# Kernel tuning notes

Measured on AMD Instinct MI355X. Metric: run time of the kernel, lower is better.

## Reference

```python
import jax, jax.numpy as jnp
import numpy as np

# irreps structure: in = 32x0e + 16x1o, hidden = 64x0e + 32x1o, out = 32x0e + 16x1o
N = 50000
S_IN, V_IN = 32, 16
S_H, V_H = 64, 32
S_OUT, V_OUT = 32, 16
INV_SQRT3 = float(1.0 / np.sqrt(3.0))  # wigner-3j for (0,1,1)/(1,0,1)/(1,1,0)
# e3nn path weights: sqrt(ir_out.dim / sum_over_paths_to_same_output(fan_in)), fan_in = mul1*mul2
PW1_S = float((1.0 / (S_IN * S_IN + V_IN * V_IN)) ** 0.5)        # sqrt(1/1280)
PW1_V = float((3.0 / (S_IN * V_IN + V_IN * S_IN)) ** 0.5)        # sqrt(3/1024)
PW2_S = float((1.0 / (S_H * S_H + V_H * V_H)) ** 0.5)            # sqrt(1/5120)
PW2_V = float((3.0 / (S_H * V_H + V_H * S_H)) ** 0.5)            # sqrt(3/4096)


def norm_act(xs, xv, bias=None, normalize=False):
    # e3nn.nn.NormActivation with sigmoid: per-irrep-channel norm, gate by sigmoid(norm [+ bias])
    ns = jnp.abs(xs)                                 # [N, S] scalar channel norms
    nv = jnp.sqrt(jnp.sum(xv * xv, axis=-1))         # [N, V] vector channel norms
    norms = jnp.concatenate([ns, nv], axis=1)        # [N, S+V]
    a = norms if bias is None else norms + bias
    f = jax.nn.sigmoid(a)
    mult = f / norms if normalize else f
    s = xs.shape[1]
    return xs * mult[:, :s], xv * mult[:, s:, None]


def fctp(xs, xv, Wsss, Wvvs, Wsvv, Wvsv, pw_s, pw_v):
    # FullyConnectedTensorProduct(x, x) restricted to 0e/1o irreps (all surviving CG paths)
    zs = pw_s * (jnp.einsum('nu,nv,uvw->nw', xs, xs, Wsss)
                 + INV_SQRT3 * jnp.einsum('nui,nvi,uvw->nw', xv, xv, Wvvs))
    zv = (pw_v * INV_SQRT3) * (jnp.einsum('nu,nvk,uvw->nwk', xs, xv, Wsvv)
                               + jnp.einsum('nuk,nv,uvw->nwk', xv, xs, Wvsv))
    return zs, zv


def setup_inputs() -> dict:
    key = jax.random.key(0)
    ks = jax.random.split(key, 11)
    return {
        'x': jax.random.normal(ks[0], (N, S_IN + 3 * V_IN), dtype=jnp.float32),
        'Wsss1': jax.random.normal(ks[1], (S_IN, S_IN, S_H), dtype=jnp.float32),
        'Wvvs1': jax.random.normal(ks[2], (V_IN, V_IN, S_H), dtype=jnp.float32),
        'Wsvv1': jax.random.normal(ks[3], (S_IN, V_IN, V_H), dtype=jnp.float32),
        'Wvsv1': jax.random.normal(ks[4], (V_IN, S_IN, V_H), dtype=jnp.float32),
        'Wsss2': jax.random.normal(ks[5], (S_H, S_H, S_OUT), dtype=jnp.float32),
        'Wvvs2': jax.random.normal(ks[6], (V_H, V_H, S_OUT), dtype=jnp.float32),
        'Wsvv2': jax.random.normal(ks[7], (S_H, V_H, V_OUT), dtype=jnp.float32),
        'Wvsv2': jax.random.normal(ks[8], (V_H, S_H, V_OUT), dtype=jnp.float32),
        'b1': 0.1 * jax.random.normal(ks[9], (S_IN + V_IN,), dtype=jnp.float32),
        'b3': 0.1 * jax.random.normal(ks[10], (S_OUT + V_OUT,), dtype=jnp.float32),
    }


def reference(x, Wsss1, Wvvs1, Wsvv1, Wvsv1, Wsss2, Wvvs2, Wsvv2, Wvsv2, b1, b3):
    xs = x[:, :S_IN]
    xv = x[:, S_IN:].reshape(-1, V_IN, 3)
    xs, xv = norm_act(xs, xv, bias=b1, normalize=False)            # non_linear_act1
    hs, hv = fctp(xs, xv, Wsss1, Wvvs1, Wsvv1, Wvsv1, PW1_S, PW1_V)  # si1
    hs, hv = norm_act(hs, hv, bias=None, normalize=True)           # normalize_and_non_linear_act2
    os_, ov = fctp(hs, hv, Wsss2, Wvvs2, Wsvv2, Wvsv2, PW2_S, PW2_V)  # si2
    os_, ov = norm_act(os_, ov, bias=b3, normalize=False)          # non_linear_act3
    return jnp.concatenate([os_, ov.reshape(-1, V_OUT * 3)], axis=1)
```

## Files before the change

### kernel.cpp

```cpp
#include <hip/hip_runtime.h>

#define NROWS 50000

typedef float f32x4 __attribute__((ext_vector_type(4)));
typedef float f32x16 __attribute__((ext_vector_type(16)));
typedef short s16x8 __attribute__((ext_vector_type(8)));
typedef _Float16 f16x8 __attribute__((ext_vector_type(8)));

#define MFMA16B(a,b,c) __builtin_amdgcn_mfma_f32_16x16x32_bf16(a, b, c, 0, 0, 0)
#define MFMA32B(a,b,c) __builtin_amdgcn_mfma_f32_32x32x16_bf16(a, b, c, 0, 0, 0)
#define MFMA32H(a,b,c) __builtin_amdgcn_mfma_f32_32x32x16_f16(a, b, c, 0, 0, 0)

#define Q1ABH 0
#define Q1ABL 81920
#define Q1CH  163840
#define Q1CL  212992
#define P2A   262144
#define P2AV  (262144 + 73728)
#define P2C   425984
#define PREPN 323584


#define LO_SCALE   2048.0f
#define LO_UNSCALE 4.8828125e-4f

__device__ __forceinline__ float sigm(float a){ return 1.0f/(1.0f+__expf(-a)); }
__device__ __forceinline__ short bfb(float f){
  __bf16 b = (__bf16)f;
  return *reinterpret_cast<short*>(&b);
}
__device__ __forceinline__ float b2f(short s){
  unsigned u = ((unsigned)(unsigned short)s) << 16;
  float f;
  __builtin_memcpy(&f, &u, 4);
  return f;
}
__device__ __forceinline__ f32x16 zero16(){
  f32x16 v;
  #pragma unroll
  for (int i = 0; i < 16; ++i) v[i] = 0.f;
  return v;
}

__global__ __launch_bounds__(256) void prep_weights(
    const float* __restrict__ Wsss1, const float* __restrict__ Wvvs1,
    const float* __restrict__ Wsvv1, const float* __restrict__ Wvsv1,
    const float* __restrict__ Wsss2, const float* __restrict__ Wvvs2,
    const float* __restrict__ Wsvv2, const float* __restrict__ Wvsv2,
    short* __restrict__ pb)
{
  const float PW1S = 0.027950849718747374f;
  const float PW2S = 0.013975424859373687f;
  const float IS3  = 0.57735026918962576f;
  int i = blockIdx.x * 256 + threadIdx.x;
  if (i >= PREPN) return;
  if (i < 131072) {
    float w;
    int hiOff, loOff;
    if (i < 81920) {
      int e = i; int j = e & 7, l = (e >> 3) & 63, st = e >> 9;
      int t = st & 1, s = st >> 1;
      int k = 16*s + 8*(l >> 5) + j, n = 32*t + (l & 31);
      if (k < 1024) { int u = k >> 5, v = k & 31; w = PW1S * Wsss1[(u*32 + v)*64 + n]; }
      else { int kk = k - 1024; int u = kk >> 4, v = kk & 15; w = PW1S * IS3 * Wvvs1[(u*16 + v)*64 + n]; }
      hiOff = Q1ABH + e; loOff = Q1ABL + e;
    } else {
      int e = i - 81920; int e2 = e & 16383;
      int j = e2 & 7, l = (e2 >> 3) & 63, s = e2 >> 9;
      int k = 16*s + 8*(l >> 5) + j, n = l & 31;
      int u = k >> 4, v = k & 15;
      w = 0.03125f * (Wsvv1[(u*16 + v)*32 + n] + Wvsv1[(v*32 + u)*32 + n]);
      hiOff = Q1CH + e; loOff = Q1CL + e;
    }
    _Float16 h = (_Float16)w;
    float r = w - (float)h;
    _Float16 lo = (_Float16)(r * LO_SCALE);
    pb[hiOff] = *reinterpret_cast<short*>(&h);
    pb[loOff] = *reinterpret_cast<short*>(&lo);
  } else {
    int e = i - 131072;
    float val; int off;
    if (e < 73728) {
      int j = e & 7, l = (e >> 3) & 63, s = e >> 9;
      int k = 16*s + 8*(l >> 5) + j, n = l & 31;
      int B = k >> 6, kb = k & 63;
      int bb = 0;
      while ((bb + 1) * (bb + 2) / 2 <= B) ++bb;
      int a = B - bb * (bb + 1) / 2;
      int u = 8*a + (kb >> 3), v = 8*bb + (kb & 7);
      float w1 = Wsss2[(u*64 + v)*32 + n];
      val = PW2S * (a == bb ? w1 : w1 + Wsss2[(v*64 + u)*32 + n]);
      off = P2A + e;
    } else if (e < 94208) {
      int e2 = e - 73728;
      int j = e2 & 7, l = (e2 >> 3) & 63, s = e2 >> 9;
      int k = 16*s + 8*(l >> 5) + j, n = l & 31;
      int B = k >> 6, kb = k & 63;
      int bb = 0;
      while ((bb + 1) * (bb + 2) / 2 <= B) ++bb;
      int a = B - bb * (bb + 1) / 2;
      int u = 8*a + (kb >> 3), v = 8*bb + (kb & 7);
      float w1 = Wvvs2[(u*32 + v)*32 + n];
      val = PW2S * IS3 * (a == bb ? w1 : w1 + Wvvs2[(v*32 + u)*32 + n]);
      off = P2AV + e2;
    } else {
      int e3 = e - 94208; int e4 = e3 & 32767;
      int j = e4 & 7, l = (e4 >> 3) & 63, s = e4 >> 9;
      int k = 32*s + 8*(l >> 4) + j, n = l & 15;
      int u = k >> 5, v = k & 31;
      val = 0.015625f * (Wsvv2[(u*32 + v)*16 + n] + Wvsv2[(v*64 + u)*16 + n]);
      off = P2C + e3;
    }
    pb[off] = bfb(val);
  }
}

__global__ __launch_bounds__(128, 4) void double_layer(
    const float* __restrict__ x,
    const float* __restrict__ b1,
    const float* __restrict__ b3,
    const short* __restrict__ pb,
    float* __restrict__ out)
{
  __shared__ __align__(16) float smem[5120];
  char* S = (char*)smem;

  const int lane = threadIdx.x & 63;
  const int wid  = __builtin_amdgcn_readfirstlane(threadIdx.x >> 6);
  const int h    = lane >> 5;
  const int r31  = lane & 31;
  const int row  = r31;
  const int grow0 = blockIdx.x * 32;
  const int xb = row * 320;
  const int hb = 10240 + row * 320;
  const int sz = ((row >> 1) & 3) << 4;
  const bool valid = (grow0 + row) < NROWS;
  const float* xrow = x + (size_t)(grow0 + row) * 80;

  if (wid == 0) {
    #pragma unroll
    for (int i = 0; i < 4; ++i) {
      float4 qv = valid ? ((const float4*)xrow)[4*h + i] : float4{0.f,0.f,0.f,0.f};
      int c0 = 16*h + 4*i;
      f32x4 o;
      o[0] = qv.x * sigm(fabsf(qv.x) + b1[c0+0]);
      o[1] = qv.y * sigm(fabsf(qv.y) + b1[c0+1]);
      o[2] = qv.z * sigm(fabsf(qv.z) + b1[c0+2]);
      o[3] = qv.w * sigm(fabsf(qv.w) + b1[c0+3]);
      *(f32x4*)(S + xb + ((64*h + 16*i) ^ sz)) = o;
    }
  } else {
    float t[24];
    #pragma unroll
    for (int i = 0; i < 6; ++i) {
      float4 qv = valid ? ((const float4*)xrow)[8 + 6*h + i] : float4{0.f,0.f,0.f,0.f};
      t[4*i] = qv.x; t[4*i+1] = qv.y; t[4*i+2] = qv.z; t[4*i+3] = qv.w;
    }
    #pragma unroll
    for (int vv = 0; vv < 8; ++vv) {
      float a0 = t[3*vv], a1 = t[3*vv+1], a2 = t[3*vv+2];
      float f = sigm(sqrtf(a0*a0 + a1*a1 + a2*a2) + b1[32 + 8*h + vv]);
      t[3*vv] = a0*f; t[3*vv+1] = a1*f; t[3*vv+2] = a2*f;
    }
    #pragma unroll
    for (int i = 0; i < 6; ++i) {
      f32x4 o; o[0] = t[4*i]; o[1] = t[4*i+1]; o[2] = t[4*i+2]; o[3] = t[4*i+3];
      *(f32x4*)(S + xb + ((128 + 96*h + 16*i) ^ sz)) = o;
    }
  }
  __syncthreads();

  if (wid == 0) {
    f32x16 aH0 = zero16(), aM0 = zero16(), aH1 = zero16(), aM1 = zero16();
    const f16x8* BH = (const f16x8*)(pb + Q1ABH);
    const f16x8* BL = (const f16x8*)(pb + Q1ABL);
    float xsv[16];
    {
      #pragma unroll
      for (int si = 0; si < 2; ++si) {
        f32x4 p0 = *(const f32x4*)(S + xb + ((64*si + 32*h) ^ sz));
        f32x4 p1 = *(const f32x4*)(S + xb + ((64*si + 32*h + 16) ^ sz));
        #pragma unroll
        for (int j = 0; j < 4; ++j) { xsv[8*si+j] = p0[j]; xsv[8*si+4+j] = p1[j]; }
      }
    }
    #pragma unroll 2
    for (int so = 0; so < 32; ++so) {
      float xu = *(const float*)(S + xb + ((4*so) ^ sz));
      #pragma unroll
      for (int si = 0; si < 2; ++si) {
        int s = 2*so + si;
        f16x8 ah, al;
        #pragma unroll
        for (int j = 0; j < 8; ++j) {
          float f = xu * xsv[8*si + j];
          _Float16 hh = (_Float16)f;
          ah[j] = hh;
          al[j] = (_Float16)((f - (float)hh) * LO_SCALE);
        }
        const f16x8* Bh = BH + (2*s)*64 + lane;
        const f16x8* Bl = BL + (2*s)*64 + lane;
        f16x8 b0 = Bh[0], b1_ = Bh[64];
        aH0 = MFMA32H(ah, b0,  aH0); aM0 = MFMA32H(al, b0,  aM0); aM0 = MFMA32H(ah, Bl[0],  aM0);
        aH1 = MFMA32H(ah, b1_, aH1); aM1 = MFMA32H(al, b1_, aM1); aM1 = MFMA32H(ah, Bl[64], aM1);
      }
    }
    {
      float pv0[8], pv1[8], pv2[8];
      f32x4 P[6];
      #pragma unroll
      for (int i = 0; i < 6; ++i) P[i] = *(const f32x4*)(S + xb + ((128 + 96*h + 16*i) ^ sz));
      #pragma unroll
      for (int j = 0; j < 8; ++j) {
        pv0[j] = P[(3*j  )>>2][(3*j  )&3];
        pv1[j] = P[(3*j+1)>>2][(3*j+1)&3];
        pv2[j] = P[(3*j+2)>>2][(3*j+2)&3];
      }
      #pragma unroll 2
      for (int s2 = 0; s2 < 16; ++s2) {
        int s = 64 + s2;
        float u0 = *(const float*)(S + xb + ((4*(32 + 3*s2    )) ^ sz));
        float u1 = *(const float*)(S + xb + ((4*(32 + 3*s2 + 1)) ^ sz));
        float u2 = *(const float*)(S + xb + ((4*(32 + 3*s2 + 2)) ^ sz));
        f16x8 ah, al;
        #pragma unroll
        for (int j = 0; j < 8; ++j) {
          float f = u0*pv0[j] + u1*pv1[j] + u2*pv2[j];
          _Float16 hh = (_Float16)f;
          ah[j] = hh;
          al[j] = (_Float16)((f - (float)hh) * LO_SCALE);
        }
        const f16x8* Bh = BH + (2*s)*64 + lane;
        const f16x8* Bl = BL + (2*s)*64 + lane;
        f16x8 b0 = Bh[0], b1_ = Bh[64];
        aH0 = MFMA32H(ah, b0,  aH0); aM0 = MFMA32H(al, b0,  aM0); aM0 = MFMA32H(ah, Bl[0],  aM0);
        aH1 = MFMA32H(ah, b1_, aH1); aM1 = MFMA32H(al, b1_, aM1); aM1 = MFMA32H(ah, Bl[64], aM1);
      }
    }
    #pragma unroll
    for (int reg = 0; reg < 16; ++reg) {
      int rowD = (reg & 3) + 8*(reg >> 2) + 4*h;
      int hbD = 10240 + rowD*320;
      int szD = ((rowD >> 1) & 3) << 4;
      float z0 = aH0[reg] + LO_UNSCALE*aM0[reg];
      float z1 = aH1[reg] + LO_UNSCALE*aM1[reg];
      *(short*)(S + hbD + ((2*r31)        ^ szD)) = bfb(copysignf(sigm(fabsf(z0)), z0));
      *(short*)(S + hbD + ((2*(32 + r31)) ^ szD)) = bfb(copysignf(sigm(fabsf(z1)), z1));
    }
  } else {
    float pv0[8], pv1[8], pv2[8];
    {
      f32x4 P[6];
      #pragma unroll
      for (int i = 0; i < 6; ++i) P[i] = *(const f32x4*)(S + xb + ((128 + 96*h + 16*i) ^ sz));
      #pragma unroll
      for (int j = 0; j < 8; ++j) {
        pv0[j] = P[(3*j  )>>2][(3*j  )&3];
        pv1[j] = P[(3*j+1)>>2][(3*j+1)&3];
        pv2[j] = P[(3*j+2)>>2][(3*j+2)&3];
      }
    }
    const f16x8* CH = (const f16x8*)(pb + Q1CH);
    const f16x8* CL = (const f16x8*)(pb + Q1CL);
    f32x16 z0v, z1v, z2v;
    {
      f32x16 cH0 = zero16(), cM0 = zero16(), cH1 = zero16(), cM1 = zero16();
      #pragma unroll 2
      for (int s = 0; s < 32; ++s) {
        float xu = *(const float*)(S + xb + ((4*s) ^ sz));
        f16x8 a0h, a0l, a1h, a1l;
        #pragma unroll
        for (int j = 0; j < 8; ++j) {
          float f0 = xu*pv0[j]; _Float16 h0 = (_Float16)f0; a0h[j] = h0; a0l[j] = (_Float16)((f0 - (float)h0)*LO_SCALE);
          float f1 = xu*pv1[j]; _Float16 h1 = (_Float16)f1; a1h[j] = h1; a1l[j] = (_Float16)((f1 - (float)h1)*LO_SCALE);
        }
        const f16x8* B0h = CH + s*64 + lane;
        const f16x8* B0l = CL + s*64 + lane;
        f16x8 t0 = B0h[0];
        cH0 = MFMA32H(a0h, t0, cH0); cM0 = MFMA32H(a0l, t0, cM0); cM0 = MFMA32H(a0h, B0l[0], cM0);
        f16x8 t1 = B0h[2048];
        cH1 = MFMA32H(a1h, t1, cH1); cM1 = MFMA32H(a1l, t1, cM1); cM1 = MFMA32H(a1h, B0l[2048], cM1);
      }
      #pragma unroll
      for (int i = 0; i < 16; ++i) { z0v[i] = cH0[i] + LO_UNSCALE*cM0[i]; z1v[i] = cH1[i] + LO_UNSCALE*cM1[i]; }
    }
    {
      f32x16 cH2 = zero16(), cM2 = zero16();
      #pragma unroll 2
      for (int s = 0; s < 32; ++s) {
        float xu = *(const float*)(S + xb + ((4*s) ^ sz));
        f16x8 a2h, a2l;
        #pragma unroll
        for (int j = 0; j < 8; ++j) {
          float f2 = xu*pv2[j]; _Float16 h2 = (_Float16)f2; a2h[j] = h2; a2l[j] = (_Float16)((f2 - (float)h2)*LO_SCALE);
        }
        const f16x8* B2h = CH + 4096 + s*64 + lane;
        const f16x8* B2l = CL + 4096 + s*64 + lane;
        f16x8 t2 = B2h[0];
        cH2 = MFMA32H(a2h, t2, cH2); cM2 = MFMA32H(a2l, t2, cM2); cM2 = MFMA32H(a2h, B2l[0], cM2);
      }
      #pragma unroll
      for (int i = 0; i < 16; ++i) z2v[i] = cH2[i] + LO_UNSCALE*cM2[i];
    }
    #pragma unroll
    for (int reg = 0; reg < 16; ++reg) {
      int rowD = (reg & 3) + 8*(reg >> 2) + 4*h;
      int hbD = 10240 + rowD*320;
      int szD = ((rowD >> 1) & 3) << 4;
      float a0 = z0v[reg], a1 = z1v[reg], a2 = z2v[reg];
      float n = sqrtf(a0*a0 + a1*a1 + a2*a2);
      float mm = sigm(n) / n;
      int ch = 64 + 3*r31;
      *(short*)(S + hbD + ((2*(ch    )) ^ szD)) = bfb(a0*mm);
      *(short*)(S + hbD + ((2*(ch + 1)) ^ szD)) = bfb(a1*mm);
      *(short*)(S + hbD + ((2*(ch + 2)) ^ szD)) = bfb(a2*mm);
    }
  }
  __syncthreads();

  if (wid == 0) {
    f32x16 acc = zero16();
    {
      const s16x8* BA = (const s16x8*)(pb + P2A);
      int step = 0;
      #pragma unroll 2
      for (int b = 0; b < 8; ++b) {
        float hsb[8];
        {
          s16x8 w = *(const s16x8*)(S + hb + ((16*b) ^ sz));
          #pragma unroll
          for (int j = 0; j < 8; ++j) hsb[j] = b2f(w[j]);
        }
        for (int a = 0; a <= b; ++a) {
          #pragma unroll
          for (int s4 = 0; s4 < 4; ++s4) {
            float hu = b2f(*(const short*)(S + hb + ((2*(8*a + 2*s4 + h)) ^ sz)));
            s16x8 av;
            #pragma unroll
            for (int j = 0; j < 8; ++j) av[j] = bfb(hu * hsb[j]);
            acc = MFMA32B(av, BA[step*64 + lane], acc);
            ++step;
          }
        }
      }
    }
    {
      const s16x8* BV = (const s16x8*)(pb + P2AV);
      int step = 0;
      #pragma unroll
      for (int b = 0; b < 4; ++b) {
        float hvb[24];
        #pragma unroll
        for (int i = 0; i < 3; ++i) {
          s16x8 w = *(const s16x8*)(S + hb + ((2*(64 + 24*b + 8*i)) ^ sz));
          #pragma unroll
          for (int j = 0; j < 8; ++j) hvb[8*i + j] = b2f(w[j]);
        }
        for (int a = 0; a <= b; ++a) {
          #pragma unroll
          for (int s4 = 0; s4 < 4; ++s4) {
            int u = 8*a + 2*s4 + h;
            float u0 = b2f(*(const short*)(S + hb + ((2*(64 + 3*u    )) ^ sz)));
            float u1 = b2f(*(const short*)(S + hb + ((2*(64 + 3*u + 1)) ^ sz)));
            float u2 = b2f(*(const short*)(S + hb + ((2*(64 + 3*u + 2)) ^ sz)));
            s16x8 av;
            #pragma unroll
            for (int j = 0; j < 8; ++j)
              av[j] = bfb(u0*hvb[3*j] + u1*hvb[3*j+1] + u2*hvb[3*j+2]);
            acc = MFMA32B(av, BV[step*64 + lane], acc);
            ++step;
          }
        }
      }
    }
    float bs = b3[r31];
    #pragma unroll
    for (int reg = 0; reg < 16; ++reg) {
      int rowD = (reg & 3) + 8*(reg >> 2) + 4*h;
      int grow = grow0 + rowD;
      if (grow < NROWS) {
        float z = acc[reg];
        out[(size_t)grow*80 + r31] = z * sigm(fabsf(z) + bs);
      }
    }
  } else {
    const int q = lane >> 4, r15 = lane & 15;
    const int rA = r15, rB = 16 + r15;
    const int hbA = 10240 + rA*320, szA = ((rA >> 1) & 3) << 4;
    const int hbB = 10240 + rB*320, szB = ((rB >> 1) & 3) << 4;
    float vvA[24], vvB[24];
    #pragma unroll
    for (int i = 0; i < 3; ++i) {
      s16x8 wa = *(const s16x8*)(S + hbA + ((128 + 48*q + 16*i) ^ szA));
      s16x8 wb = *(const s16x8*)(S + hbB + ((128 + 48*q + 16*i) ^ szB));
      #pragma unroll
      for (int j = 0; j < 8; ++j) { vvA[8*i+j] = b2f(wa[j]); vvB[8*i+j] = b2f(wb[j]); }
    }
    f32x4 ac00 = {0.f,0.f,0.f,0.f}, ac01 = {0.f,0.f,0.f,0.f};
    f32x4 ac10 = {0.f,0.f,0.f,0.f}, ac11 = {0.f,0.f,0.f,0.f};
    f32x4 ac20 = {0.f,0.f,0.f,0.f}, ac21 = {0.f,0.f,0.f,0.f};
    const s16x8* BC = (const s16x8*)(pb + P2C);
    #pragma unroll 2
    for (int s = 0; s < 64; ++s) {
      float huA = b2f(*(const short*)(S + hbA + ((2*s) ^ szA)));
      float huB = b2f(*(const short*)(S + hbB + ((2*s) ^ szB)));
      s16x8 aA0, aA1, aA2, aB0, aB1, aB2;
      #pragma unroll
      for (int j = 0; j < 8; ++j) {
        aA0[j] = bfb(huA*vvA[3*j  ]); aA1[j] = bfb(huA*vvA[3*j+1]); aA2[j] = bfb(huA*vvA[3*j+2]);
        aB0[j] = bfb(huB*vvB[3*j  ]); aB1[j] = bfb(huB*vvB[3*j+1]); aB2[j] = bfb(huB*vvB[3*j+2]);
      }
      s16x8 B0 = BC[s*64 + lane];
      s16x8 B1 = BC[4096 + s*64 + lane];
      s16x8 B2 = BC[8192 + s*64 + lane];
      ac00 = MFMA16B(aA0, B0, ac00); ac01 = MFMA16B(aB0, B0, ac01);
      ac10 = MFMA16B(aA1, B1, ac10); ac11 = MFMA16B(aB1, B1, ac11);
      ac20 = MFMA16B(aA2, B2, ac20); ac21 = MFMA16B(aB2, B2, ac21);
    }
    float bv = b3[32 + r15];
    #pragma unroll
    for (int r = 0; r < 4; ++r) {
      int gA = grow0 + 4*q + r;
      if (gA < NROWS) {
        float z0 = ac00[r], z1 = ac10[r], z2 = ac20[r];
        float gg = sigm(sqrtf(z0*z0 + z1*z1 + z2*z2) + bv);
        out[(size_t)gA*80 + 32 + 3*r15    ] = z0*gg;
        out[(size_t)gA*80 + 32 + 3*r15 + 1] = z1*gg;
        out[(size_t)gA*80 + 32 + 3*r15 + 2] = z2*gg;
      }
      int gB = grow0 + 16 + 4*q + r;
      if (gB < NROWS) {
        float z0 = ac01[r], z1 = ac11[r], z2 = ac21[r];
        float gg = sigm(sqrtf(z0*z0 + z1*z1 + z2*z2) + bv);
        out[(size_t)gB*80 + 32 + 3*r15    ] = z0*gg;
        out[(size_t)gB*80 + 32 + 3*r15 + 1] = z1*gg;
        out[(size_t)gB*80 + 32 + 3*r15 + 2] = z2*gg;
      }
    }
  }
}

extern "C" void kernel_launch(void* const* d_in, const int* in_sizes, int n_in,
                              void* d_out, int out_size, void* d_ws, size_t ws_size,
                              hipStream_t stream) {
  const float* x     = (const float*)d_in[0];
  const float* Wsss1 = (const float*)d_in[1];
  const float* Wvvs1 = (const float*)d_in[2];
  const float* Wsvv1 = (const float*)d_in[3];
  const float* Wvsv1 = (const float*)d_in[4];
  const float* Wsss2 = (const float*)d_in[5];
  const float* Wvvs2 = (const float*)d_in[6];
  const float* Wsvv2 = (const float*)d_in[7];
  const float* Wvsv2 = (const float*)d_in[8];
  const float* b1    = (const float*)d_in[9];
  const float* b3    = (const float*)d_in[10];
  float* out = (float*)d_out;
  short* pb  = (short*)d_ws;

  hipLaunchKernelGGL(prep_weights, dim3((PREPN + 255)/256), dim3(256), 0, stream,
                     Wsss1, Wvvs1, Wsvv1, Wvsv1, Wsss2, Wvvs2, Wsvv2, Wvsv2, pb);
  hipLaunchKernelGGL(double_layer, dim3((NROWS + 31)/32), dim3(128), 0, stream,
                     x, b1, b3, pb, out);
}
```

Baseline: 116.2 us.

## Split fused kernel into separate layer-1 and layer-2 kernels via global hidden buffer

Splits the fused two-layer kernel into two launches. The first layer now runs on 16-row tiles with 16x16x32 f16 MFMAs and a repacked weight layout, and writes the bf16 hidden activations to a workspace buffer in global memory. The second kernel loads that buffer into shared memory and runs the unchanged layer-2 path on 32-row tiles. The aim is more, smaller blocks and lower register and LDS pressure for layer 1, paid for with an extra launch and a global round trip of the hidden state.

```diff
diff --git a/kernel.cpp b/kernel.cpp
--- a/kernel.cpp
+++ b/kernel.cpp
@@ -1,6 +1,8 @@
 #include <hip/hip_runtime.h>
 
 #define NROWS 50000
+#define NT16  (NROWS / 16)
+#define NT32  ((NROWS + 31) / 32)
 
 typedef float f32x4 __attribute__((ext_vector_type(4)));
 typedef float f32x16 __attribute__((ext_vector_type(16)));
@@ -9,7 +11,7 @@
 
 #define MFMA16B(a,b,c) __builtin_amdgcn_mfma_f32_16x16x32_bf16(a, b, c, 0, 0, 0)
 #define MFMA32B(a,b,c) __builtin_amdgcn_mfma_f32_32x32x16_bf16(a, b, c, 0, 0, 0)
-#define MFMA32H(a,b,c) __builtin_amdgcn_mfma_f32_32x32x16_f16(a, b, c, 0, 0, 0)
+#define MFMAH(a,b,c)   __builtin_amdgcn_mfma_f32_16x16x32_f16(a, b, c, 0, 0, 0)
 
 #define Q1ABH 0
 #define Q1ABL 81920
@@ -19,8 +21,10 @@
 #define P2AV  (262144 + 73728)
 #define P2C   425984
 #define PREPN 323584
-
-
+#define HWSOFF 524288
+
+
+#define XSTR 17
 #define LO_SCALE   2048.0f
 #define LO_UNSCALE 4.8828125e-4f
 
@@ -59,15 +63,16 @@
     int hiOff, loOff;
     if (i < 81920) {
       int e = i; int j = e & 7, l = (e >> 3) & 63, st = e >> 9;
-      int t = st & 1, s = st >> 1;
-      int k = 16*s + 8*(l >> 5) + j, n = 32*t + (l & 31);
+      int t = st & 3, s = st >> 2;
+      int k = 32*s + 8*(l >> 4) + j, n = 16*t + (l & 15);
       if (k < 1024) { int u = k >> 5, v = k & 31; w = PW1S * Wsss1[(u*32 + v)*64 + n]; }
       else { int kk = k - 1024; int u = kk >> 4, v = kk & 15; w = PW1S * IS3 * Wvvs1[(u*16 + v)*64 + n]; }
       hiOff = Q1ABH + e; loOff = Q1ABL + e;
     } else {
       int e = i - 81920; int e2 = e & 16383;
-      int j = e2 & 7, l = (e2 >> 3) & 63, s = e2 >> 9;
-      int k = 16*s + 8*(l >> 5) + j, n = l & 31;
+      int j = e2 & 7, l = (e2 >> 3) & 63, st = e2 >> 9;
+      int t = st & 1, s = st >> 1;
+      int k = 32*s + 8*(l >> 4) + j, n = 16*t + (l & 15);
       int u = k >> 4, v = k & 15;
       w = 0.03125f * (Wsvv1[(u*16 + v)*32 + n] + Wvsv1[(v*32 + u)*32 + n]);
       hiOff = Q1CH + e; loOff = Q1CL + e;
@@ -77,244 +82,240 @@
     _Float16 lo = (_Float16)(r * LO_SCALE);
     pb[hiOff] = *reinterpret_cast<short*>(&h);
     pb[loOff] = *reinterpret_cast<short*>(&lo);
+  } else if (i < 204800) {
+    int e = i - 131072;
+    int j = e & 7, l = (e >> 3) & 63, s = e >> 9;
+    int k = 16*s + 8*(l >> 5) + j, n = l & 31;
+    int B = k >> 6, kb = k & 63;
+    int bb = 0;
+    while ((bb + 1) * (bb + 2) / 2 <= B) ++bb;
+    int a = B - bb * (bb + 1) / 2;
+    int u = 8*a + (kb >> 3), v = 8*bb + (kb & 7);
+    float w1 = Wsss2[(u*64 + v)*32 + n];
+    float val = PW2S * (a == bb ? w1 : w1 + Wsss2[(v*64 + u)*32 + n]);
+    pb[P2A + e] = bfb(val);
+  } else if (i < 225280) {
+    int e2 = i - 204800;
+    int j = e2 & 7, l = (e2 >> 3) & 63, s = e2 >> 9;
+    int k = 16*s + 8*(l >> 5) + j, n = l & 31;
+    int B = k >> 6, kb = k & 63;
+    int bb = 0;
+    while ((bb + 1) * (bb + 2) / 2 <= B) ++bb;
+    int a = B - bb * (bb + 1) / 2;
+    int u = 8*a + (kb >> 3), v = 8*bb + (kb & 7);
+    float w1 = Wvvs2[(u*32 + v)*32 + n];
+    float val = PW2S * IS3 * (a == bb ? w1 : w1 + Wvvs2[(v*32 + u)*32 + n]);
+    pb[P2AV + e2] = bfb(val);
   } else {
-    int e = i - 131072;
-    float val; int off;
-    if (e < 73728) {
-      int j = e & 7, l = (e >> 3) & 63, s = e >> 9;
-      int k = 16*s + 8*(l >> 5) + j, n = l & 31;
-      int B = k >> 6, kb = k & 63;
-      int bb = 0;
-      while ((bb + 1) * (bb + 2) / 2 <= B) ++bb;
-      int a = B - bb * (bb + 1) / 2;
-      int u = 8*a + (kb >> 3), v = 8*bb + (kb & 7);
-      float w1 = Wsss2[(u*64 + v)*32 + n];
-      val = PW2S * (a == bb ? w1 : w1 + Wsss2[(v*64 + u)*32 + n]);
-      off = P2A + e;
-    } else if (e < 94208) {
-      int e2 = e - 73728;
-      int j = e2 & 7, l = (e2 >> 3) & 63, s = e2 >> 9;
-      int k = 16*s + 8*(l >> 5) + j, n = l & 31;
-      int B = k >> 6, kb = k & 63;
-      int bb = 0;
-      while ((bb + 1) * (bb + 2) / 2 <= B) ++bb;
-      int a = B - bb * (bb + 1) / 2;
-      int u = 8*a + (kb >> 3), v = 8*bb + (kb & 7);
-      float w1 = Wvvs2[(u*32 + v)*32 + n];
-      val = PW2S * IS3 * (a == bb ? w1 : w1 + Wvvs2[(v*32 + u)*32 + n]);
-      off = P2AV + e2;
-    } else {
-      int e3 = e - 94208; int e4 = e3 & 32767;
-      int j = e4 & 7, l = (e4 >> 3) & 63, s = e4 >> 9;
-      int k = 32*s + 8*(l >> 4) + j, n = l & 15;
-      int u = k >> 5, v = k & 31;
-      val = 0.015625f * (Wsvv2[(u*32 + v)*16 + n] + Wvsv2[(v*64 + u)*16 + n]);
-      off = P2C + e3;
-    }
-    pb[off] = bfb(val);
+    int e3 = i - 225280; int e4 = e3 & 32767;
+    int j = e4 & 7, l = (e4 >> 3) & 63, s = e4 >> 9;
+    int k = 32*s + 8*(l >> 4) + j, n = l & 15;
+    int u = k >> 5, v = k & 31;
+    float val = 0.015625f * (Wsvv2[(u*32 + v)*16 + n] + Wvsv2[(v*64 + u)*16 + n]);
+    pb[P2C + e3] = bfb(val);
   }
 }
 
-__global__ __launch_bounds__(128, 4) void double_layer(
+__global__ __launch_bounds__(128, 4) void double_layer_l1(
     const float* __restrict__ x,
     const float* __restrict__ b1,
+    const short* __restrict__ pb,
+    char* __restrict__ hws)
+{
+  __shared__ float smem[1360];
+
+  const int lane = threadIdx.x & 63;
+  const int wid  = __builtin_amdgcn_readfirstlane(threadIdx.x >> 6);
+  const int q = lane >> 4, r15 = lane & 15;
+  const int g = r15;
+  const int row = blockIdx.x * 16 + r15;
+  const float* xrow = x + (size_t)row * 80;
+
+  if (wid == 0) {
+    const float4* xq = (const float4*)xrow;
+    float4 va = xq[2*q], vb2 = xq[2*q + 1];
+    float t[8] = {va.x, va.y, va.z, va.w, vb2.x, vb2.y, vb2.z, vb2.w};
+    #pragma unroll
+    for (int j = 0; j < 8; ++j) {
+      int c = 8*q + j;
+      smem[c*XSTR + r15] = t[j] * sigm(fabsf(t[j]) + b1[c]);
+    }
+  } else {
+    const float4* xq = (const float4*)xrow;
+    float4 va = xq[8 + 3*q], vb2 = xq[9 + 3*q], vc = xq[10 + 3*q];
+    float t[12] = {va.x, va.y, va.z, va.w, vb2.x, vb2.y, vb2.z, vb2.w, vc.x, vc.y, vc.z, vc.w};
+    #pragma unroll
+    for (int i = 0; i < 4; ++i) {
+      int v = 4*q + i;
+      float a0 = t[3*i], a1 = t[3*i+1], a2 = t[3*i+2];
+      float f = sigm(sqrtf(a0*a0 + a1*a1 + a2*a2) + b1[32 + v]);
+      smem[(32+3*v  )*XSTR + r15] = a0*f;
+      smem[(32+3*v+1)*XSTR + r15] = a1*f;
+      smem[(32+3*v+2)*XSTR + r15] = a2*f;
+    }
+  }
+  __syncthreads();
+
+  const int vb = 8*(q & 1);
+
+  if (wid == 0) {
+    float xvp[8];
+    #pragma unroll
+    for (int j = 0; j < 8; ++j) xvp[j] = smem[(8*q + j)*XSTR + g];
+    f32x4 aH0={0.f,0.f,0.f,0.f}, aH1={0.f,0.f,0.f,0.f}, aH2={0.f,0.f,0.f,0.f}, aH3={0.f,0.f,0.f,0.f};
+    f32x4 aM0={0.f,0.f,0.f,0.f}, aM1={0.f,0.f,0.f,0.f}, aM2={0.f,0.f,0.f,0.f}, aM3={0.f,0.f,0.f,0.f};
+    const f16x8* BH = (const f16x8*)(pb + Q1ABH);
+    const f16x8* BL = (const f16x8*)(pb + Q1ABL);
+    #pragma unroll 4
+    for (int s = 0; s < 32; ++s) {
+      float xu = smem[s*XSTR + g];
+      f16x8 ah, al;
+      #pragma unroll
+      for (int j = 0; j < 8; ++j) {
+        float f = xu * xvp[j];
+        _Float16 hh = (_Float16)f;
+        ah[j] = hh;
+        al[j] = (_Float16)((f - (float)hh) * LO_SCALE);
+      }
+      const f16x8* Bh = BH + s*256 + lane;
+      const f16x8* Bl = BL + s*256 + lane;
+      f16x8 b0=Bh[0], b1_=Bh[64], b2=Bh[128], b3_=Bh[192];
+      aH0 = MFMAH(ah, b0,  aH0); aM0 = MFMAH(al, b0,  aM0); aM0 = MFMAH(ah, Bl[0],   aM0);
+      aH1 = MFMAH(ah, b1_, aH1); aM1 = MFMAH(al, b1_, aM1); aM1 = MFMAH(ah, Bl[64],  aM1);
+      aH2 = MFMAH(ah, b2,  aH2); aM2 = MFMAH(al, b2,  aM2); aM2 = MFMAH(ah, Bl[128], aM2);
+      aH3 = MFMAH(ah, b3_, aH3); aM3 = MFMAH(al, b3_, aM3); aM3 = MFMAH(ah, Bl[192], aM3);
+    }
+    float pv0[8], pv1[8], pv2[8];
+    #pragma unroll
+    for (int j = 0; j < 8; ++j) {
+      pv0[j] = smem[(32 + 3*(vb+j)    )*XSTR + g];
+      pv1[j] = smem[(32 + 3*(vb+j) + 1)*XSTR + g];
+      pv2[j] = smem[(32 + 3*(vb+j) + 2)*XSTR + g];
+    }
+    #pragma unroll 2
+    for (int s2 = 0; s2 < 8; ++s2) {
+      int u = 2*s2 + (q >> 1);
+      float u0 = smem[(32+3*u  )*XSTR + g];
+      float u1 = smem[(32+3*u+1)*XSTR + g];
+      float u2 = smem[(32+3*u+2)*XSTR + g];
+      f16x8 ah, al;
+      #pragma unroll
+      for (int j = 0; j < 8; ++j) {
+        float f = u0*pv0[j] + u1*pv1[j] + u2*pv2[j];
+        _Float16 hh = (_Float16)f;
+        ah[j] = hh;
+        al[j] = (_Float16)((f - (float)hh) * LO_SCALE);
+      }
+      const f16x8* Bh = BH + (32+s2)*256 + lane;
+      const f16x8* Bl = BL + (32+s2)*256 + lane;
+      f16x8 b0=Bh[0], b1_=Bh[64], b2=Bh[128], b3_=Bh[192];
+      aH0 = MFMAH(ah, b0,  aH0); aM0 = MFMAH(al, b0,  aM0); aM0 = MFMAH(ah, Bl[0],   aM0);
+      aH1 = MFMAH(ah, b1_, aH1); aM1 = MFMAH(al, b1_, aM1); aM1 = MFMAH(ah, Bl[64],  aM1);
+      aH2 = MFMAH(ah, b2,  aH2); aM2 = MFMAH(al, b2,  aM2); aM2 = MFMAH(ah, Bl[128], aM2);
+      aH3 = MFMAH(ah, b3_, aH3); aM3 = MFMAH(al, b3_, aM3); aM3 = MFMAH(ah, Bl[192], aM3);
+    }
+    #pragma unroll
+    for (int r = 0; r < 4; ++r) {
+      int rw = 4*q + r;
+      size_t base = (size_t)(blockIdx.x*16 + rw) * 320;
+      int szD = ((rw >> 1) & 3) << 4;
+      float z;
+      z = aH0[r] + LO_UNSCALE*aM0[r]; *(short*)(hws + base + ((2*(     r15)) ^ szD)) = bfb(copysignf(sigm(fabsf(z)), z));
+      z = aH1[r] + LO_UNSCALE*aM1[r]; *(short*)(hws + base + ((2*(16 + r15)) ^ szD)) = bfb(copysignf(sigm(fabsf(z)), z));
+      z = aH2[r] + LO_UNSCALE*aM2[r]; *(short*)(hws + base + ((2*(32 + r15)) ^ szD)) = bfb(copysignf(sigm(fabsf(z)), z));
+      z = aH3[r] + LO_UNSCALE*aM3[r]; *(short*)(hws + base + ((2*(48 + r15)) ^ szD)) = bfb(copysignf(sigm(fabsf(z)), z));
+    }
+  } else {
+    float pv0[8], pv1[8], pv2[8];
+    #pragma unroll
+    for (int j = 0; j < 8; ++j) {
+      pv0[j] = smem[(32 + 3*(vb+j)    )*XSTR + g];
+      pv1[j] = smem[(32 + 3*(vb+j) + 1)*XSTR + g];
+      pv2[j] = smem[(32 + 3*(vb+j) + 2)*XSTR + g];
+    }
+    f32x4 cH00={0.f,0.f,0.f,0.f}, cH01={0.f,0.f,0.f,0.f}, cH10={0.f,0.f,0.f,0.f},
+          cH11={0.f,0.f,0.f,0.f}, cH20={0.f,0.f,0.f,0.f}, cH21={0.f,0.f,0.f,0.f};
+    f32x4 cM00={0.f,0.f,0.f,0.f}, cM01={0.f,0.f,0.f,0.f}, cM10={0.f,0.f,0.f,0.f},
+          cM11={0.f,0.f,0.f,0.f}, cM20={0.f,0.f,0.f,0.f}, cM21={0.f,0.f,0.f,0.f};
+    const f16x8* CH = (const f16x8*)(pb + Q1CH);
+    const f16x8* CL = (const f16x8*)(pb + Q1CL);
+    #pragma unroll 2
+    for (int s = 0; s < 16; ++s) {
+      float xu = smem[(2*s + (q >> 1))*XSTR + g];
+      f16x8 a0h,a0l,a1h,a1l,a2h,a2l;
+      #pragma unroll
+      for (int j = 0; j < 8; ++j) {
+        float f0 = xu*pv0[j]; _Float16 h0=(_Float16)f0; a0h[j]=h0; a0l[j]=(_Float16)((f0-(float)h0)*LO_SCALE);
+        float f1 = xu*pv1[j]; _Float16 h1=(_Float16)f1; a1h[j]=h1; a1l[j]=(_Float16)((f1-(float)h1)*LO_SCALE);
+        float f2 = xu*pv2[j]; _Float16 h2=(_Float16)f2; a2h[j]=h2; a2l[j]=(_Float16)((f2-(float)h2)*LO_SCALE);
+      }
+      const f16x8* B0h = CH + s*128 + lane;
+      const f16x8* B0l = CL + s*128 + lane;
+      const f16x8* B1h = B0h + 2048, *B1l = B0l + 2048;
+      const f16x8* B2h = B0h + 4096, *B2l = B0l + 4096;
+      f16x8 t0=B0h[0], t1=B0h[64], t2=B1h[0], t3=B1h[64], t4=B2h[0], t5=B2h[64];
+      cH00 = MFMAH(a0h, t0, cH00); cM00 = MFMAH(a0l, t0, cM00); cM00 = MFMAH(a0h, B0l[0],  cM00);
+      cH01 = MFMAH(a0h, t1, cH01); cM01 = MFMAH(a0l, t1, cM01); cM01 = MFMAH(a0h, B0l[64], cM01);
+      cH10 = MFMAH(a1h, t2, cH10); cM10 = MFMAH(a1l, t2, cM10); cM10 = MFMAH(a1h, B1l[0],  cM10);
+      cH11 = MFMAH(a1h, t3, cH11); cM11 = MFMAH(a1l, t3, cM11); cM11 = MFMAH(a1h, B1l[64], cM11);
+      cH20 = MFMAH(a2h, t4, cH20); cM20 = MFMAH(a2l, t4, cM20); cM20 = MFMAH(a2h, B2l[0],  cM20);
+      cH21 = MFMAH(a2h, t5, cH21); cM21 = MFMAH(a2l, t5, cM21); cM21 = MFMAH(a2h, B2l[64], cM21);
+    }
+    #pragma unroll
+    for (int r = 0; r < 4; ++r) {
+      int rw = 4*q + r;
+      size_t base = (size_t)(blockIdx.x*16 + rw) * 320;
+      int szD = ((rw >> 1) & 3) << 4;
+      {
+        float z0 = cH00[r] + LO_UNSCALE*cM00[r];
+        float z1 = cH10[r] + LO_UNSCALE*cM10[r];
+        float z2 = cH20[r] + LO_UNSCALE*cM20[r];
+        float n = sqrtf(z0*z0 + z1*z1 + z2*z2);
+        float mm = sigm(n) / n;
+        int ch = 64 + 3*r15;
+        *(short*)(hws + base + ((2*(ch    )) ^ szD)) = bfb(z0*mm);
+        *(short*)(hws + base + ((2*(ch + 1)) ^ szD)) = bfb(z1*mm);
+        *(short*)(hws + base + ((2*(ch + 2)) ^ szD)) = bfb(z2*mm);
+      }
+      {
+        float z0 = cH01[r] + LO_UNSCALE*cM01[r];
+        float z1 = cH11[r] + LO_UNSCALE*cM11[r];
+        float z2 = cH21[r] + LO_UNSCALE*cM21[r];
+        float n = sqrtf(z0*z0 + z1*z1 + z2*z2);
+        float mm = sigm(n) / n;
+        int ch = 64 + 3*(16 + r15);
+        *(short*)(hws + base + ((2*(ch    )) ^ szD)) = bfb(z0*mm);
+        *(short*)(hws + base + ((2*(ch + 1)) ^ szD)) = bfb(z1*mm);
+        *(short*)(hws + base + ((2*(ch + 2)) ^ szD)) = bfb(z2*mm);
+      }
+    }
+  }
+}
+
+__global__ __launch_bounds__(128, 4) void double_layer_l2(
     const float* __restrict__ b3,
     const short* __restrict__ pb,
+    const short* __restrict__ hws,
     float* __restrict__ out)
 {
   __shared__ __align__(16) float smem[5120];
   char* S = (char*)smem;
-
   const int lane = threadIdx.x & 63;
   const int wid  = __builtin_amdgcn_readfirstlane(threadIdx.x >> 6);
   const int h    = lane >> 5;
   const int r31  = lane & 31;
+  const int grow0 = blockIdx.x * 32;
   const int row  = r31;
-  const int grow0 = blockIdx.x * 32;
-  const int xb = row * 320;
   const int hb = 10240 + row * 320;
   const int sz = ((row >> 1) & 3) << 4;
-  const bool valid = (grow0 + row) < NROWS;
-  const float* xrow = x + (size_t)(grow0 + row) * 80;
-
-  if (wid == 0) {
-    #pragma unroll
-    for (int i = 0; i < 4; ++i) {
-      float4 qv = valid ? ((const float4*)xrow)[4*h + i] : float4{0.f,0.f,0.f,0.f};
-      int c0 = 16*h + 4*i;
-      f32x4 o;
-      o[0] = qv.x * sigm(fabsf(qv.x) + b1[c0+0]);
-      o[1] = qv.y * sigm(fabsf(qv.y) + b1[c0+1]);
-      o[2] = qv.z * sigm(fabsf(qv.z) + b1[c0+2]);
-      o[3] = qv.w * sigm(fabsf(qv.w) + b1[c0+3]);
-      *(f32x4*)(S + xb + ((64*h + 16*i) ^ sz)) = o;
-    }
-  } else {
-    float t[24];
-    #pragma unroll
-    for (int i = 0; i < 6; ++i) {
-      float4 qv = valid ? ((const float4*)xrow)[8 + 6*h + i] : float4{0.f,0.f,0.f,0.f};
-      t[4*i] = qv.x; t[4*i+1] = qv.y; t[4*i+2] = qv.z; t[4*i+3] = qv.w;
-    }
-    #pragma unroll
-    for (int vv = 0; vv < 8; ++vv) {
-      float a0 = t[3*vv], a1 = t[3*vv+1], a2 = t[3*vv+2];
-      float f = sigm(sqrtf(a0*a0 + a1*a1 + a2*a2) + b1[32 + 8*h + vv]);
-      t[3*vv] = a0*f; t[3*vv+1] = a1*f; t[3*vv+2] = a2*f;
-    }
-    #pragma unroll
-    for (int i = 0; i < 6; ++i) {
-      f32x4 o; o[0] = t[4*i]; o[1] = t[4*i+1]; o[2] = t[4*i+2]; o[3] = t[4*i+3];
-      *(f32x4*)(S + xb + ((128 + 96*h + 16*i) ^ sz)) = o;
-    }
-  }
-  __syncthreads();
-
-  if (wid == 0) {
-    f32x16 aH0 = zero16(), aM0 = zero16(), aH1 = zero16(), aM1 = zero16();
-    const f16x8* BH = (const f16x8*)(pb + Q1ABH);
-    const f16x8* BL = (const f16x8*)(pb + Q1ABL);
-    float xsv[16];
-    {
-      #pragma unroll
-      for (int si = 0; si < 2; ++si) {
-        f32x4 p0 = *(const f32x4*)(S + xb + ((64*si + 32*h) ^ sz));
-        f32x4 p1 = *(const f32x4*)(S + xb + ((64*si + 32*h + 16) ^ sz));
-        #pragma unroll
-        for (int j = 0; j < 4; ++j) { xsv[8*si+j] = p0[j]; xsv[8*si+4+j] = p1[j]; }
-      }
-    }
-    #pragma unroll 2
-    for (int so = 0; so < 32; ++so) {
-      float xu = *(const float*)(S + xb + ((4*so) ^ sz));
-      #pragma unroll
-      for (int si = 0; si < 2; ++si) {
-        int s = 2*so + si;
-        f16x8 ah, al;
-        #pragma unroll
-        for (int j = 0; j < 8; ++j) {
-          float f = xu * xsv[8*si + j];
-          _Float16 hh = (_Float16)f;
-          ah[j] = hh;
-          al[j] = (_Float16)((f - (float)hh) * LO_SCALE);
-        }
-        const f16x8* Bh = BH + (2*s)*64 + lane;
-        const f16x8* Bl = BL + (2*s)*64 + lane;
-        f16x8 b0 = Bh[0], b1_ = Bh[64];
-        aH0 = MFMA32H(ah, b0,  aH0); aM0 = MFMA32H(al, b0,  aM0); aM0 = MFMA32H(ah, Bl[0],  aM0);
-        aH1 = MFMA32H(ah, b1_, aH1); aM1 = MFMA32H(al, b1_, aM1); aM1 = MFMA32H(ah, Bl[64], aM1);
-      }
-    }
-    {
-      float pv0[8], pv1[8], pv2[8];
-      f32x4 P[6];
-      #pragma unroll
-      for (int i = 0; i < 6; ++i) P[i] = *(const f32x4*)(S + xb + ((128 + 96*h + 16*i) ^ sz));
-      #pragma unroll
-      for (int j = 0; j < 8; ++j) {
-        pv0[j] = P[(3*j  )>>2][(3*j  )&3];
-        pv1[j] = P[(3*j+1)>>2][(3*j+1)&3];
-        pv2[j] = P[(3*j+2)>>2][(3*j+2)&3];
-      }
-      #pragma unroll 2
-      for (int s2 = 0; s2 < 16; ++s2) {
-        int s = 64 + s2;
-        float u0 = *(const float*)(S + xb + ((4*(32 + 3*s2    )) ^ sz));
-        float u1 = *(const float*)(S + xb + ((4*(32 + 3*s2 + 1)) ^ sz));
-        float u2 = *(const float*)(S + xb + ((4*(32 + 3*s2 + 2)) ^ sz));
-        f16x8 ah, al;
-        #pragma unroll
-        for (int j = 0; j < 8; ++j) {
-          float f = u0*pv0[j] + u1*pv1[j] + u2*pv2[j];
-          _Float16 hh = (_Float16)f;
-          ah[j] = hh;
-          al[j] = (_Float16)((f - (float)hh) * LO_SCALE);
-        }
-        const f16x8* Bh = BH + (2*s)*64 + lane;
-        const f16x8* Bl = BL + (2*s)*64 + lane;
-        f16x8 b0 = Bh[0], b1_ = Bh[64];
-        aH0 = MFMA32H(ah, b0,  aH0); aM0 = MFMA32H(al, b0,  aM0); aM0 = MFMA32H(ah, Bl[0],  aM0);
-        aH1 = MFMA32H(ah, b1_, aH1); aM1 = MFMA32H(al, b1_, aM1); aM1 = MFMA32H(ah, Bl[64], aM1);
-      }
-    }
-    #pragma unroll
-    for (int reg = 0; reg < 16; ++reg) {
-      int rowD = (reg & 3) + 8*(reg >> 2) + 4*h;
-      int hbD = 10240 + rowD*320;
-      int szD = ((rowD >> 1) & 3) << 4;
-      float z0 = aH0[reg] + LO_UNSCALE*aM0[reg];
-      float z1 = aH1[reg] + LO_UNSCALE*aM1[reg];
-      *(short*)(S + hbD + ((2*r31)        ^ szD)) = bfb(copysignf(sigm(fabsf(z0)), z0));
-      *(short*)(S + hbD + ((2*(32 + r31)) ^ szD)) = bfb(copysignf(sigm(fabsf(z1)), z1));
-    }
-  } else {
-    float pv0[8], pv1[8], pv2[8];
-    {
-      f32x4 P[6];
-      #pragma unroll
-      for (int i = 0; i < 6; ++i) P[i] = *(const f32x4*)(S + xb + ((128 + 96*h + 16*i) ^ sz));
-      #pragma unroll
-      for (int j = 0; j < 8; ++j) {
-        pv0[j] = P[(3*j  )>>2][(3*j  )&3];
-        pv1[j] = P[(3*j+1)>>2][(3*j+1)&3];
-        pv2[j] = P[(3*j+2)>>2][(3*j+2)&3];
-      }
-    }
-    const f16x8* CH = (const f16x8*)(pb + Q1CH);
-    const f16x8* CL = (const f16x8*)(pb + Q1CL);
-    f32x16 z0v, z1v, z2v;
-    {
-      f32x16 cH0 = zero16(), cM0 = zero16(), cH1 = zero16(), cM1 = zero16();
-      #pragma unroll 2
-      for (int s = 0; s < 32; ++s) {
-        float xu = *(const float*)(S + xb + ((4*s) ^ sz));
-        f16x8 a0h, a0l, a1h, a1l;
-        #pragma unroll
-        for (int j = 0; j < 8; ++j) {
-          float f0 = xu*pv0[j]; _Float16 h0 = (_Float16)f0; a0h[j] = h0; a0l[j] = (_Float16)((f0 - (float)h0)*LO_SCALE);
-          float f1 = xu*pv1[j]; _Float16 h1 = (_Float16)f1; a1h[j] = h1; a1l[j] = (_Float16)((f1 - (float)h1)*LO_SCALE);
-        }
-        const f16x8* B0h = CH + s*64 + lane;
-        const f16x8* B0l = CL + s*64 + lane;
-        f16x8 t0 = B0h[0];
-        cH0 = MFMA32H(a0h, t0, cH0); cM0 = MFMA32H(a0l, t0, cM0); cM0 = MFMA32H(a0h, B0l[0], cM0);
-        f16x8 t1 = B0h[2048];
-        cH1 = MFMA32H(a1h, t1, cH1); cM1 = MFMA32H(a1l, t1, cM1); cM1 = MFMA32H(a1h, B0l[2048], cM1);
-      }
-      #pragma unroll
-      for (int i = 0; i < 16; ++i) { z0v[i] = cH0[i] + LO_UNSCALE*cM0[i]; z1v[i] = cH1[i] + LO_UNSCALE*cM1[i]; }
-    }
-    {
-      f32x16 cH2 = zero16(), cM2 = zero16();
-      #pragma unroll 2
-      for (int s = 0; s < 32; ++s) {
-        float xu = *(const float*)(S + xb + ((4*s) ^ sz));
-        f16x8 a2h, a2l;
-        #pragma unroll
-        for (int j = 0; j < 8; ++j) {
-          float f2 = xu*pv2[j]; _Float16 h2 = (_Float16)f2; a2h[j] = h2; a2l[j] = (_Float16)((f2 - (float)h2)*LO_SCALE);
-        }
-        const f16x8* B2h = CH + 4096 + s*64 + lane;
-        const f16x8* B2l = CL + 4096 + s*64 + lane;
-        f16x8 t2 = B2h[0];
-        cH2 = MFMA32H(a2h, t2, cH2); cM2 = MFMA32H(a2l, t2, cM2); cM2 = MFMA32H(a2h, B2l[0], cM2);
-      }
-      #pragma unroll
-      for (int i = 0; i < 16; ++i) z2v[i] = cH2[i] + LO_UNSCALE*cM2[i];
-    }
-    #pragma unroll
-    for (int reg = 0; reg < 16; ++reg) {
-      int rowD = (reg & 3) + 8*(reg >> 2) + 4*h;
-      int hbD = 10240 + rowD*320;
-      int szD = ((rowD >> 1) & 3) << 4;
-      float a0 = z0v[reg], a1 = z1v[reg], a2 = z2v[reg];
-      float n = sqrtf(a0*a0 + a1*a1 + a2*a2);
-      float mm = sigm(n) / n;
-      int ch = 64 + 3*r31;
-      *(short*)(S + hbD + ((2*(ch    )) ^ szD)) = bfb(a0*mm);
-      *(short*)(S + hbD + ((2*(ch + 1)) ^ szD)) = bfb(a1*mm);
-      *(short*)(S + hbD + ((2*(ch + 2)) ^ szD)) = bfb(a2*mm);
-    }
+
+  {
+    const s16x8* src = (const s16x8*)(hws + (size_t)blockIdx.x * 5120);
+    s16x8* dst = (s16x8*)(S + 10240);
+    int tid = threadIdx.x;
+    #pragma unroll
+    for (int i = 0; i < 5; ++i)
+      dst[tid + 128*i] = src[tid + 128*i];
   }
   __syncthreads();
 
@@ -456,9 +457,12 @@
   const float* b3    = (const float*)d_in[10];
   float* out = (float*)d_out;
   short* pb  = (short*)d_ws;
+  short* hws = pb + HWSOFF;
 
   hipLaunchKernelGGL(prep_weights, dim3((PREPN + 255)/256), dim3(256), 0, stream,
                      Wsss1, Wvvs1, Wsvv1, Wvsv1, Wsss2, Wvvs2, Wsvv2, Wvsv2, pb);
-  hipLaunchKernelGGL(double_layer, dim3((NROWS + 31)/32), dim3(128), 0, stream,
-                     x, b1, b3, pb, out);
-}
+  hipLaunchKernelGGL(double_layer_l1, dim3(NT16), dim3(128), 0, stream,
+                     x, b1, pb, (char*)hws);
+  hipLaunchKernelGGL(double_layer_l2, dim3(NT32), dim3(128), 0, stream,
+                     b3, pb, hws, out);
+}
```

New measurement: 129.3 us. 1.11x slower.
